# Kernel optimization log

Measured on AMD Instinct MI355X. Metric: run time of the kernel, lower is better.

The kernel has to match this reference:

```python
import jax, jax.numpy as jnp
import numpy as np

EMBED_DIM = 512
NUM_TYPES = 26
PER_TYPE = 128
NUM_CODES = NUM_TYPES * PER_TYPE
COMMIT = 0.25
TEMP = 0.07
N_TOKENS = 32768
SAMPLED_PER_TYPE = int(0.1 * PER_TYPE)  # 12


def _normalize(v, axis=-1):
    # matches F.normalize(p=2) with eps clamp
    return v / jnp.clip(jnp.linalg.norm(v, axis=axis, keepdims=True), 1e-12)


def setup_inputs() -> dict:
    key = jax.random.key(0)
    k1, k2, k3, k4 = jax.random.split(key, 4)
    x = jax.random.normal(k1, (N_TOKENS, EMBED_DIM), jnp.float32)
    Q = jax.random.randint(k2, (N_TOKENS,), 0, NUM_TYPES)
    initrange = 1.0 / EMBED_DIM
    emb = jax.random.uniform(k3, (NUM_CODES, EMBED_DIM), jnp.float32, -initrange, initrange)
    emb = _normalize(emb)  # mirrors _initialize_embeddings
    # deterministic stand-in for torch.randperm(num_per_type)[:sampled_num]
    perm = jax.random.permutation(k4, PER_TYPE)[:SAMPLED_PER_TYPE]
    sampled_indices = (jnp.arange(NUM_TYPES)[:, None] * PER_TYPE + perm[None, :]).reshape(-1)
    return {"x": x, "embeddings": emb, "Q": Q, "sampled_indices": sampled_indices}


def _code_indices(xn, embeddings, Q):
    # full [N, num_codes] squared distances, then select the 128-code slab of
    # each token's PTM type and argmin within it (equivalent to the per-type loop)
    d = ((xn ** 2).sum(-1, keepdims=True)
         + (embeddings ** 2).sum(-1)[None, :]
         - 2.0 * (xn @ embeddings.T))                      # [N, NUM_CODES]
    d = d.reshape(xn.shape[0], NUM_TYPES, PER_TYPE)
    d_sel = jnp.take_along_axis(d, Q[:, None, None], axis=1)[:, 0, :]  # [N, PER_TYPE]
    return jnp.argmin(d_sel, axis=1) + Q * PER_TYPE


def _uniform_loss(embeddings, sampled_indices):
    ne = _normalize(embeddings)
    se = ne[sampled_indices]                               # [S, D]
    sim = se @ se.T                                        # [S, S]
    labels = sampled_indices // PER_TYPE
    pos = (labels[None, :] == labels[:, None]).astype(jnp.float32)
    S = sampled_indices.shape[0]
    eye = jnp.eye(S, dtype=bool)
    sim = jnp.where(eye, -jnp.inf, sim)
    sim_exp = jnp.exp(sim / TEMP)                          # exp(-inf) = 0 kills diagonal
    sum_exp = sim_exp.sum(axis=1)
    pos_sum = (sim_exp * pos).sum(axis=1)
    return -jnp.log(pos_sum / sum_exp).mean()


def reference(x, embeddings, Q, sampled_indices):
    xn = _normalize(x)
    idx = _code_indices(xn, embeddings, Q)
    quantized = _normalize(embeddings[idx])
    q_latent = jnp.mean((quantized - jax.lax.stop_gradient(xn)) ** 2)
    e_latent = jnp.mean((xn - jax.lax.stop_gradient(quantized)) ** 2)
    loss = q_latent + COMMIT * e_latent
    uloss = _uniform_loss(embeddings, sampled_indices)
    out = xn + jax.lax.stop_gradient(quantized - xn)       # straight-through
    return out, loss, uloss, idx
```

## Files before the change

kernel.cpp:

```cpp
#include <hip/hip_runtime.h>
#include <math.h>

#define NTOK   32768
#define DIM    512
#define NTYPES 26
#define PT     128
#define NCODES 3328
#define NSAMP  312
#define INV_TEMP (1.0f / 0.07f)
#define MAXTILES 24

typedef __attribute__((ext_vector_type(8))) short short8;
typedef __attribute__((ext_vector_type(4))) float floatx4;

__device__ __forceinline__ void f2bf2(float f, unsigned short& h, unsigned short& l) {
    unsigned u = __float_as_uint(f);
    unsigned hb = (u + 0x7fffu + ((u >> 16) & 1u)) >> 16;
    h = (unsigned short)hb;
    float hf = __uint_as_float(hb << 16);
    float r = f - hf;
    unsigned u2 = __float_as_uint(r);
    l = (unsigned short)((u2 + 0x7fffu + ((u2 >> 16) & 1u)) >> 16);
}

__device__ __forceinline__ void cvt8(float4 a, float4 b, short8& h, short8& l) {
    union { short8 v; unsigned short u[8]; } H, L;
    f2bf2(a.x, H.u[0], L.u[0]); f2bf2(a.y, H.u[1], L.u[1]);
    f2bf2(a.z, H.u[2], L.u[2]); f2bf2(a.w, H.u[3], L.u[3]);
    f2bf2(b.x, H.u[4], L.u[4]); f2bf2(b.y, H.u[5], L.u[5]);
    f2bf2(b.z, H.u[6], L.u[6]); f2bf2(b.w, H.u[7], L.u[7]);
    h = H.v; l = L.v;
}

__device__ __forceinline__ void stage2(const unsigned short* g, unsigned short* l) {
    __builtin_amdgcn_global_load_lds((const __attribute__((address_space(1))) void*)g,
                                     (__attribute__((address_space(3))) void*)l, 16, 0, 0);
    __builtin_amdgcn_global_load_lds((const __attribute__((address_space(1))) void*)(g + 512),
                                     (__attribute__((address_space(3))) void*)(l + 512), 16, 0, 0);
}

__global__ __launch_bounds__(256) void k_emb(const float* __restrict__ emb,
                                             unsigned short* __restrict__ Bhg,
                                             unsigned short* __restrict__ Blg,
                                             float* __restrict__ sume,
                                             float* __restrict__ rinv,
                                             int* __restrict__ counts,
                                             float* __restrict__ accg) {
    int tid = threadIdx.x;
    if (blockIdx.x == 0) {
        if (tid < NTYPES) counts[tid] = 0;
        if (tid == 32) accg[0] = 0.0f;
        if (tid == 33) accg[1] = 0.0f;
    }
    int wv = tid >> 6, lane = tid & 63;
    int c = blockIdx.x * 4 + wv;
    const float4* row = (const float4*)(emb + (size_t)c * DIM);
    float4 v0 = row[lane * 2], v1 = row[lane * 2 + 1];
    float s = v0.x*v0.x + v0.y*v0.y + v0.z*v0.z + v0.w*v0.w
            + v1.x*v1.x + v1.y*v1.y + v1.z*v1.z + v1.w*v1.w;
    for (int m = 32; m; m >>= 1) s += __shfl_xor(s, m);
    if (lane == 0) {
        sume[c] = s;
        rinv[c] = 1.0f / fmaxf(sqrtf(s), 1e-12f);
    }
    union { short8 v; unsigned short u[8]; } hh, ll;
    f2bf2(v0.x, hh.u[0], ll.u[0]); f2bf2(v0.y, hh.u[1], ll.u[1]);
    f2bf2(v0.z, hh.u[2], ll.u[2]); f2bf2(v0.w, hh.u[3], ll.u[3]);
    f2bf2(v1.x, hh.u[4], ll.u[4]); f2bf2(v1.y, hh.u[5], ll.u[5]);
    f2bf2(v1.z, hh.u[6], ll.u[6]); f2bf2(v1.w, hh.u[7], ll.u[7]);
    int qq  = c >> 7;
    int n   = c & 127;
    int ni  = n >> 4, lcc = n & 15;
    int ks2 = lane >> 2, q4d = lane & 3;
    size_t dst = (size_t)qq * (PT * DIM)
               + (size_t)(((ks2 * 8 + ni) * 64 + q4d * 16 + lcc) * 8);
    *(short8*)(Bhg + dst) = hh.v;
    *(short8*)(Blg + dst) = ll.v;
}

__global__ __launch_bounds__(256) void k_hist(const int* __restrict__ Q,
                                              int* __restrict__ counts,
                                              int* __restrict__ rank) {
    __shared__ int lbin[NTYPES];
    __shared__ int lbase[NTYPES];
    int tid = threadIdx.x;
    if (tid < NTYPES) lbin[tid] = 0;
    __syncthreads();
    int t = blockIdx.x * 256 + tid;
    int qt = Q[t];
    int lr = atomicAdd(&lbin[qt], 1);
    __syncthreads();
    if (tid < NTYPES) lbase[tid] = atomicAdd(&counts[tid], lbin[tid]);
    __syncthreads();
    rank[t] = lbase[qt] + lr;
}

__global__ __launch_bounds__(256) void k_scatter(const int* __restrict__ Q,
                                                 const int* __restrict__ counts,
                                                 const int* __restrict__ rank,
                                                 int* __restrict__ order,
                                                 int* __restrict__ offsg) {
    __shared__ int offs[NTYPES];
    int tid = threadIdx.x;
    if (tid == 0) {
        int a = 0;
        for (int i = 0; i < NTYPES; i++) {
            offs[i] = a;
            if (blockIdx.x == 0) offsg[i] = a;
            a += counts[i];
        }
        if (blockIdx.x == 0) offsg[NTYPES] = a;
    }
    __syncthreads();
    int t = blockIdx.x * 256 + tid;
    order[offs[Q[t]] + rank[t]] = t;
}

#define KSTEP(S, NSTR, AC, AN, RESTAGE, LOADA)                                   \
  {                                                                              \
    __builtin_amdgcn_sched_barrier(0);                                           \
    asm volatile("s_waitcnt vmcnt(" NSTR ")" ::: "memory");                      \
    __builtin_amdgcn_s_barrier();                                                \
    __builtin_amdgcn_sched_barrier(0);                                           \
    if (RESTAGE) {                                                               \
      stage2(bhg + ((S) + 1) * 4096 + stoff, &Bls[((S) + 1) & 1][0][ldoff]);     \
      stage2(blg + ((S) + 1) * 4096 + stoff, &Bls[((S) + 1) & 1][1][ldoff]);     \
    }                                                                            \
    __builtin_amdgcn_sched_barrier(0);                                           \
    if (LOADA) {                                                                 \
      AN[0] = *(const float4*)(ap0 + ((S) + 1) * 32);                            \
      AN[1] = *(const float4*)(ap0 + ((S) + 1) * 32 + 4);                        \
      AN[2] = *(const float4*)(ap1 + ((S) + 1) * 32);                            \
      AN[3] = *(const float4*)(ap1 + ((S) + 1) * 32 + 4);                        \
    }                                                                            \
    {                                                                            \
      float4 r0a = AC[0], r0b = AC[1], r1a = AC[2], r1b = AC[3];                 \
      ps0 = fmaf(r0a.x, r0a.x, fmaf(r0a.y, r0a.y, fmaf(r0a.z, r0a.z, fmaf(r0a.w, r0a.w, ps0)))); \
      ps0 = fmaf(r0b.x, r0b.x, fmaf(r0b.y, r0b.y, fmaf(r0b.z, r0b.z, fmaf(r0b.w, r0b.w, ps0)))); \
      ps1 = fmaf(r1a.x, r1a.x, fmaf(r1a.y, r1a.y, fmaf(r1a.z, r1a.z, fmaf(r1a.w, r1a.w, ps1)))); \
      ps1 = fmaf(r1b.x, r1b.x, fmaf(r1b.y, r1b.y, fmaf(r1b.z, r1b.z, fmaf(r1b.w, r1b.w, ps1)))); \
      short8 ah0, al0, ah1, al1;                                                 \
      cvt8(r0a, r0b, ah0, al0);                                                  \
      cvt8(r1a, r1b, ah1, al1);                                                  \
      short8 bhf[4], blf[4];                                                     \
      _Pragma("unroll")                                                          \
      for (int ni = 0; ni < 4; ni++) {                                           \
        bhf[ni] = *(const short8*)&Bls[(S) & 1][0][(wn4 + ni) * 512 + lane8];    \
        blf[ni] = *(const short8*)&Bls[(S) & 1][1][(wn4 + ni) * 512 + lane8];    \
      }                                                                          \
      _Pragma("unroll")                                                          \
      for (int ni = 0; ni < 4; ni++) {                                           \
        acc[0][ni] = __builtin_amdgcn_mfma_f32_16x16x32_bf16(ah0, bhf[ni], acc[0][ni], 0, 0, 0); \
        acc[0][ni] = __builtin_amdgcn_mfma_f32_16x16x32_bf16(ah0, blf[ni], acc[0][ni], 0, 0, 0); \
        acc[0][ni] = __builtin_amdgcn_mfma_f32_16x16x32_bf16(al0, bhf[ni], acc[0][ni], 0, 0, 0); \
        acc[1][ni] = __builtin_amdgcn_mfma_f32_16x16x32_bf16(ah1, bhf[ni], acc[1][ni], 0, 0, 0); \
        acc[1][ni] = __builtin_amdgcn_mfma_f32_16x16x32_bf16(ah1, blf[ni], acc[1][ni], 0, 0, 0); \
        acc[1][ni] = __builtin_amdgcn_mfma_f32_16x16x32_bf16(al1, bhf[ni], acc[1][ni], 0, 0, 0); \
      }                                                                          \
    }                                                                            \
  }

__global__ __launch_bounds__(256, 3) void k_main(const float* __restrict__ x,
                                                 const float* __restrict__ emb,
                                                 const unsigned short* __restrict__ Bhg,
                                                 const unsigned short* __restrict__ Blg,
                                                 const int* __restrict__ order,
                                                 const int* __restrict__ offsg,
                                                 const float* __restrict__ sume,
                                                 const float* __restrict__ rinv,
                                                 float* __restrict__ outbuf,
                                                 float* __restrict__ idxout,
                                                 float* __restrict__ accg) {
    int q = blockIdx.x;
    int tile = blockIdx.y;
    int base = offsg[q];
    int cnt = offsg[q + 1] - base;
    int tstart = tile * 64;
    if (tstart >= cnt) return;
    int nt = min(64, cnt - tstart);

    __shared__ unsigned short Bls[2][2][4096];
    __shared__ int   toks_s[64];
    __shared__ float sume_s[128];
    __shared__ float rinv_s[128];
    __shared__ float redv[64][2];
    __shared__ int   redi[64][2];
    __shared__ int   bestc[64];

    int tid = threadIdx.x;
    int lane = tid & 63;
    int wv = tid >> 6;
    int wm = wv & 1, wn = wv >> 1;
    int lc = lane & 15, q4 = lane >> 4;
    int wn4 = wn * 4, lane8 = lane * 8;
    int stoff = wv * 1024 + lane8;
    int ldoff = wv * 1024;

    if (tid < 64) toks_s[tid] = order[base + tstart + min(tid, nt - 1)];
    if (tid < 128) {
        sume_s[tid] = sume[q * PT + tid];
        rinv_s[tid] = rinv[q * PT + tid];
    }

    int row0 = wm * 32 + lc;
    int tok0 = order[base + tstart + min(row0, nt - 1)];
    int tok1 = order[base + tstart + min(row0 + 16, nt - 1)];
    const float* ap0 = x + (size_t)tok0 * DIM + q4 * 8;
    const float* ap1 = x + (size_t)tok1 * DIM + q4 * 8;

    const unsigned short* bhg = Bhg + (size_t)q * (PT * DIM);
    const unsigned short* blg = Blg + (size_t)q * (PT * DIM);

    floatx4 acc[2][4];
#pragma unroll
    for (int mi = 0; mi < 2; mi++)
#pragma unroll
        for (int ni = 0; ni < 4; ni++)
            acc[mi][ni] = (floatx4){0.f, 0.f, 0.f, 0.f};
    float ps0 = 0.f, ps1 = 0.f;
    float4 Aa[4], Ab[4];

    stage2(bhg + stoff, &Bls[0][0][ldoff]);
    stage2(blg + stoff, &Bls[0][1][ldoff]);
    __builtin_amdgcn_sched_barrier(0);
    Aa[0] = *(const float4*)(ap0);     Aa[1] = *(const float4*)(ap0 + 4);
    Aa[2] = *(const float4*)(ap1);     Aa[3] = *(const float4*)(ap1 + 4);
    __builtin_amdgcn_sched_barrier(0);
    stage2(bhg + 4096 + stoff, &Bls[1][0][ldoff]);
    stage2(blg + 4096 + stoff, &Bls[1][1][ldoff]);
    asm volatile("s_waitcnt lgkmcnt(0)" ::: "memory");

    KSTEP(0,  "8", Aa, Ab, 0, 1)
    KSTEP(1,  "4", Ab, Aa, 1, 1)
    KSTEP(2,  "4", Aa, Ab, 1, 1)
    KSTEP(3,  "4", Ab, Aa, 1, 1)
    KSTEP(4,  "4", Aa, Ab, 1, 1)
    KSTEP(5,  "4", Ab, Aa, 1, 1)
    KSTEP(6,  "4", Aa, Ab, 1, 1)
    KSTEP(7,  "4", Ab, Aa, 1, 1)
    KSTEP(8,  "4", Aa, Ab, 1, 1)
    KSTEP(9,  "4", Ab, Aa, 1, 1)
    KSTEP(10, "4", Aa, Ab, 1, 1)
    KSTEP(11, "4", Ab, Aa, 1, 1)
    KSTEP(12, "4", Aa, Ab, 1, 1)
    KSTEP(13, "4", Ab, Aa, 1, 1)
    KSTEP(14, "4", Aa, Ab, 1, 1)
    KSTEP(15, "4", Ab, Aa, 0, 0)

    ps0 += __shfl_xor(ps0, 16); ps0 += __shfl_xor(ps0, 32);
    ps1 += __shfl_xor(ps1, 16); ps1 += __shfl_xor(ps1, 32);
    float rn0 = 1.0f / fmaxf(sqrtf(ps0), 1e-12f);
    float rn1 = 1.0f / fmaxf(sqrtf(ps1), 1e-12f);

#pragma unroll
    for (int mi = 0; mi < 2; mi++) {
#pragma unroll
        for (int r = 0; r < 4; r++) {
            int rowrel = q4 * 4 + r;
            float rn = __shfl(mi == 0 ? rn0 : rn1, rowrel);
            float rn2v = -2.0f * rn;
            float bv = 1e30f; int bc = 0;
#pragma unroll
            for (int ni = 0; ni < 4; ni++) {
                int n = wn * 64 + ni * 16 + lc;
                float d = fmaf(rn2v, acc[mi][ni][r], sume_s[n]);
                if (d < bv) { bv = d; bc = n; }
            }
#pragma unroll
            for (int mk = 1; mk <= 8; mk <<= 1) {
                float ov = __shfl_xor(bv, mk);
                int oc = __shfl_xor(bc, mk);
                if (ov < bv || (ov == bv && oc < bc)) { bv = ov; bc = oc; }
            }
            int m = wm * 32 + mi * 16 + rowrel;
            if (lc == 0) { redv[m][wn] = bv; redi[m][wn] = bc; }
        }
    }
    __syncthreads();

    if (tid < 64) {
        float v0 = redv[tid][0], v1 = redv[tid][1];
        int c = (v1 < v0) ? redi[tid][1] : redi[tid][0];
        float bvv = fminf(v0, v1);
        bestc[tid] = c;
        float term = 0.0f;
        if (tid < nt) {
            idxout[toks_s[tid]] = (float)(q * PT + c);
            term = 2.0f - (sume_s[c] - bvv) * rinv_s[c];
        }
        for (int mk = 32; mk; mk >>= 1) term += __shfl_xor(term, mk);
        if (tid == 0) atomicAdd(&accg[0], term);
    }
    __syncthreads();

    for (int t = wv; t < nt; t += 4) {
        int c = bestc[t];
        int gt = toks_s[t];
        float rv = rinv_s[c];
        const float4* er = (const float4*)(emb + (size_t)(q * PT + c) * DIM);
        float4* orow = (float4*)(outbuf + (size_t)gt * DIM);
#pragma unroll
        for (int s2 = 0; s2 < 2; s2++) {
            float4 ev = er[lane * 2 + s2];
            orow[lane * 2 + s2] = make_float4(ev.x * rv, ev.y * rv, ev.z * rv, ev.w * rv);
        }
    }
}

__global__ __launch_bounds__(256) void k_uloss(const float* __restrict__ emb,
                                               const int* __restrict__ samp,
                                               const float* __restrict__ rinv,
                                               float* __restrict__ accg) {
    __shared__ float rs[4], rp[4];
    int i = blockIdx.x;
    int tid = threadIdx.x;
    int lane = tid & 63, wv = tid >> 6;
    int ci = samp[i];
    float rvi = rinv[ci];
    int labi = ci >> 7;
    const float4* ri = (const float4*)(emb + (size_t)ci * DIM);
    float4 e0 = ri[lane * 2], e1 = ri[lane * 2 + 1];
    float sE = 0.0f, pE = 0.0f;
    for (int j0 = wv; j0 < NSAMP; j0 += 16) {
        float d[4]; int cj[4]; bool val[4];
#pragma unroll
        for (int u = 0; u < 4; u++) {
            int j = j0 + u * 4;
            val[u] = (j < NSAMP) && (j != i);
            int js = val[u] ? j : 0;
            cj[u] = samp[js];
            const float4* rj = (const float4*)(emb + (size_t)cj[u] * DIM);
            float4 f0 = rj[lane * 2], f1 = rj[lane * 2 + 1];
            d[u] = e0.x*f0.x + e0.y*f0.y + e0.z*f0.z + e0.w*f0.w
                 + e1.x*f1.x + e1.y*f1.y + e1.z*f1.z + e1.w*f1.w;
        }
#pragma unroll
        for (int mk = 32; mk; mk >>= 1)
#pragma unroll
            for (int u = 0; u < 4; u++) d[u] += __shfl_xor(d[u], mk);
#pragma unroll
        for (int u = 0; u < 4; u++) {
            float ex = val[u] ? expf(d[u] * rvi * rinv[cj[u]] * INV_TEMP) : 0.0f;
            sE += ex;
            if (val[u] && (cj[u] >> 7) == labi) pE += ex;
        }
    }
    if (lane == 0) { rs[wv] = sE; rp[wv] = pE; }
    __syncthreads();
    if (tid == 0) {
        float S = rs[0] + rs[1] + rs[2] + rs[3];
        float P = rp[0] + rp[1] + rp[2] + rp[3];
        atomicAdd(&accg[1], logf(S) - logf(P));
    }
}

__global__ void k_final(const float* __restrict__ accg, float* __restrict__ lossp) {
    lossp[0] = (1.25f / ((float)NTOK * (float)DIM)) * accg[0];
    lossp[1] = accg[1] / (float)NSAMP;
}

extern "C" void kernel_launch(void* const* d_in, const int* in_sizes, int n_in,
                              void* d_out, int out_size, void* d_ws, size_t ws_size,
                              hipStream_t stream) {
    const float* x   = (const float*)d_in[0];
    const float* emb = (const float*)d_in[1];
    const int* Q     = (const int*)d_in[2];
    const int* samp  = (const int*)d_in[3];

    float* out    = (float*)d_out;
    float* lossp  = out + (size_t)NTOK * DIM;
    float* idxout = out + (size_t)NTOK * DIM + 2;

    unsigned short* Bhg = (unsigned short*)d_ws;
    unsigned short* Blg = Bhg + (size_t)NCODES * DIM;
    float* sume  = (float*)(Blg + (size_t)NCODES * DIM);
    float* rinv  = sume + NCODES;
    int* counts  = (int*)(rinv + NCODES);
    int* offsg   = counts + NTYPES;
    int* rank    = offsg + NTYPES + 1;
    int* order   = rank + NTOK;
    float* accg  = (float*)(order + NTOK);

    k_emb<<<NCODES / 4, 256, 0, stream>>>(emb, Bhg, Blg, sume, rinv, counts, accg);
    k_hist<<<NTOK / 256, 256, 0, stream>>>(Q, counts, rank);
    k_scatter<<<NTOK / 256, 256, 0, stream>>>(Q, counts, rank, order, offsg);
    dim3 gmain(NTYPES, MAXTILES);
    k_main<<<gmain, 256, 0, stream>>>(x, emb, Bhg, Blg, order, offsg, sume, rinv, out, idxout, accg);
    k_uloss<<<NSAMP, 256, 0, stream>>>(emb, samp, rinv, accg);
    k_final<<<1, 1, 0, stream>>>(accg, lossp);
}
```

Baseline: 209.1 us.

## Halve token tile to 32 rows and deepen A-prefetch to two steps ahead

Shrinks each block's token tile from 64 to 32 rows, so every wave computes one 16-row MFMA fragment instead of two. This doubles the maximum number of tiles per type and raises the launch-bounds occupancy hint from 3 to 4 blocks. The A-operand loads move to a triple-buffered scheme that prefetches two k-steps ahead, and the vmcnt waits are retuned to match. The aim is more blocks and lower register pressure to hide latency and balance uneven per-type token counts. The cost is that each staged B slab is reused by half as many tokens, doubling codebook traffic through LDS and L2.

```diff
diff --git a/kernel.cpp b/kernel.cpp
--- a/kernel.cpp
+++ b/kernel.cpp
@@ -8,7 +8,7 @@
 #define NCODES 3328
 #define NSAMP  312
 #define INV_TEMP (1.0f / 0.07f)
-#define MAXTILES 24
+#define MAXTILES 48
 
 typedef __attribute__((ext_vector_type(8))) short short8;
 typedef __attribute__((ext_vector_type(4))) float floatx4;
@@ -116,32 +116,27 @@
     order[offs[Q[t]] + rank[t]] = t;
 }
 
-#define KSTEP(S, NSTR, AC, AN, RESTAGE, LOADA)                                   \
+#define KSTEP(S, NSTR, AC, AF, DOSTAGE, DOLOADA)                                 \
   {                                                                              \
     __builtin_amdgcn_sched_barrier(0);                                           \
     asm volatile("s_waitcnt vmcnt(" NSTR ")" ::: "memory");                      \
     __builtin_amdgcn_s_barrier();                                                \
     __builtin_amdgcn_sched_barrier(0);                                           \
-    if (RESTAGE) {                                                               \
+    if (DOSTAGE) {                                                               \
       stage2(bhg + ((S) + 1) * 4096 + stoff, &Bls[((S) + 1) & 1][0][ldoff]);     \
       stage2(blg + ((S) + 1) * 4096 + stoff, &Bls[((S) + 1) & 1][1][ldoff]);     \
     }                                                                            \
+    if (DOLOADA) {                                                               \
+      AF[0] = *(const float4*)(ap + ((S) + 2) * 32);                             \
+      AF[1] = *(const float4*)(ap + ((S) + 2) * 32 + 4);                         \
+    }                                                                            \
     __builtin_amdgcn_sched_barrier(0);                                           \
-    if (LOADA) {                                                                 \
-      AN[0] = *(const float4*)(ap0 + ((S) + 1) * 32);                            \
-      AN[1] = *(const float4*)(ap0 + ((S) + 1) * 32 + 4);                        \
-      AN[2] = *(const float4*)(ap1 + ((S) + 1) * 32);                            \
-      AN[3] = *(const float4*)(ap1 + ((S) + 1) * 32 + 4);                        \
-    }                                                                            \
     {                                                                            \
-      float4 r0a = AC[0], r0b = AC[1], r1a = AC[2], r1b = AC[3];                 \
-      ps0 = fmaf(r0a.x, r0a.x, fmaf(r0a.y, r0a.y, fmaf(r0a.z, r0a.z, fmaf(r0a.w, r0a.w, ps0)))); \
-      ps0 = fmaf(r0b.x, r0b.x, fmaf(r0b.y, r0b.y, fmaf(r0b.z, r0b.z, fmaf(r0b.w, r0b.w, ps0)))); \
-      ps1 = fmaf(r1a.x, r1a.x, fmaf(r1a.y, r1a.y, fmaf(r1a.z, r1a.z, fmaf(r1a.w, r1a.w, ps1)))); \
-      ps1 = fmaf(r1b.x, r1b.x, fmaf(r1b.y, r1b.y, fmaf(r1b.z, r1b.z, fmaf(r1b.w, r1b.w, ps1)))); \
-      short8 ah0, al0, ah1, al1;                                                 \
-      cvt8(r0a, r0b, ah0, al0);                                                  \
-      cvt8(r1a, r1b, ah1, al1);                                                  \
+      float4 a0 = AC[0], a1 = AC[1];                                             \
+      ps = fmaf(a0.x, a0.x, fmaf(a0.y, a0.y, fmaf(a0.z, a0.z, fmaf(a0.w, a0.w, ps)))); \
+      ps = fmaf(a1.x, a1.x, fmaf(a1.y, a1.y, fmaf(a1.z, a1.z, fmaf(a1.w, a1.w, ps)))); \
+      short8 ah, al;                                                             \
+      cvt8(a0, a1, ah, al);                                                      \
       short8 bhf[4], blf[4];                                                     \
       _Pragma("unroll")                                                          \
       for (int ni = 0; ni < 4; ni++) {                                           \
@@ -150,17 +145,14 @@
       }                                                                          \
       _Pragma("unroll")                                                          \
       for (int ni = 0; ni < 4; ni++) {                                           \
-        acc[0][ni] = __builtin_amdgcn_mfma_f32_16x16x32_bf16(ah0, bhf[ni], acc[0][ni], 0, 0, 0); \
-        acc[0][ni] = __builtin_amdgcn_mfma_f32_16x16x32_bf16(ah0, blf[ni], acc[0][ni], 0, 0, 0); \
-        acc[0][ni] = __builtin_amdgcn_mfma_f32_16x16x32_bf16(al0, bhf[ni], acc[0][ni], 0, 0, 0); \
-        acc[1][ni] = __builtin_amdgcn_mfma_f32_16x16x32_bf16(ah1, bhf[ni], acc[1][ni], 0, 0, 0); \
-        acc[1][ni] = __builtin_amdgcn_mfma_f32_16x16x32_bf16(ah1, blf[ni], acc[1][ni], 0, 0, 0); \
-        acc[1][ni] = __builtin_amdgcn_mfma_f32_16x16x32_bf16(al1, bhf[ni], acc[1][ni], 0, 0, 0); \
+        acc[ni] = __builtin_amdgcn_mfma_f32_16x16x32_bf16(ah, bhf[ni], acc[ni], 0, 0, 0); \
+        acc[ni] = __builtin_amdgcn_mfma_f32_16x16x32_bf16(ah, blf[ni], acc[ni], 0, 0, 0); \
+        acc[ni] = __builtin_amdgcn_mfma_f32_16x16x32_bf16(al, bhf[ni], acc[ni], 0, 0, 0); \
       }                                                                          \
     }                                                                            \
   }
 
-__global__ __launch_bounds__(256, 3) void k_main(const float* __restrict__ x,
+__global__ __launch_bounds__(256, 4) void k_main(const float* __restrict__ x,
                                                  const float* __restrict__ emb,
                                                  const unsigned short* __restrict__ Bhg,
                                                  const unsigned short* __restrict__ Blg,
@@ -175,17 +167,17 @@
     int tile = blockIdx.y;
     int base = offsg[q];
     int cnt = offsg[q + 1] - base;
-    int tstart = tile * 64;
+    int tstart = tile * 32;
     if (tstart >= cnt) return;
-    int nt = min(64, cnt - tstart);
+    int nt = min(32, cnt - tstart);
 
     __shared__ unsigned short Bls[2][2][4096];
-    __shared__ int   toks_s[64];
+    __shared__ int   toks_s[32];
     __shared__ float sume_s[128];
     __shared__ float rinv_s[128];
-    __shared__ float redv[64][2];
-    __shared__ int   redi[64][2];
-    __shared__ int   bestc[64];
+    __shared__ float redv[32][2];
+    __shared__ int   redi[32][2];
+    __shared__ int   bestc[32];
 
     int tid = threadIdx.x;
     int lane = tid & 63;
@@ -196,89 +188,75 @@
     int stoff = wv * 1024 + lane8;
     int ldoff = wv * 1024;
 
-    if (tid < 64) toks_s[tid] = order[base + tstart + min(tid, nt - 1)];
+    if (tid < 32) toks_s[tid] = order[base + tstart + min(tid, nt - 1)];
     if (tid < 128) {
         sume_s[tid] = sume[q * PT + tid];
         rinv_s[tid] = rinv[q * PT + tid];
     }
 
-    int row0 = wm * 32 + lc;
-    int tok0 = order[base + tstart + min(row0, nt - 1)];
-    int tok1 = order[base + tstart + min(row0 + 16, nt - 1)];
-    const float* ap0 = x + (size_t)tok0 * DIM + q4 * 8;
-    const float* ap1 = x + (size_t)tok1 * DIM + q4 * 8;
+    int rowA = wm * 16 + lc;
+    int tokA = order[base + tstart + min(rowA, nt - 1)];
+    const float* ap = x + (size_t)tokA * DIM + q4 * 8;
 
     const unsigned short* bhg = Bhg + (size_t)q * (PT * DIM);
     const unsigned short* blg = Blg + (size_t)q * (PT * DIM);
 
-    floatx4 acc[2][4];
-#pragma unroll
-    for (int mi = 0; mi < 2; mi++)
-#pragma unroll
-        for (int ni = 0; ni < 4; ni++)
-            acc[mi][ni] = (floatx4){0.f, 0.f, 0.f, 0.f};
-    float ps0 = 0.f, ps1 = 0.f;
-    float4 Aa[4], Ab[4];
+    floatx4 acc[4];
+#pragma unroll
+    for (int ni = 0; ni < 4; ni++) acc[ni] = (floatx4){0.f, 0.f, 0.f, 0.f};
+    float ps = 0.f;
+    float4 Aa[2], Ab[2], Ac[2];
 
     stage2(bhg + stoff, &Bls[0][0][ldoff]);
     stage2(blg + stoff, &Bls[0][1][ldoff]);
     __builtin_amdgcn_sched_barrier(0);
-    Aa[0] = *(const float4*)(ap0);     Aa[1] = *(const float4*)(ap0 + 4);
-    Aa[2] = *(const float4*)(ap1);     Aa[3] = *(const float4*)(ap1 + 4);
-    __builtin_amdgcn_sched_barrier(0);
-    stage2(bhg + 4096 + stoff, &Bls[1][0][ldoff]);
-    stage2(blg + 4096 + stoff, &Bls[1][1][ldoff]);
-    asm volatile("s_waitcnt lgkmcnt(0)" ::: "memory");
-
-    KSTEP(0,  "8", Aa, Ab, 0, 1)
-    KSTEP(1,  "4", Ab, Aa, 1, 1)
-    KSTEP(2,  "4", Aa, Ab, 1, 1)
-    KSTEP(3,  "4", Ab, Aa, 1, 1)
-    KSTEP(4,  "4", Aa, Ab, 1, 1)
-    KSTEP(5,  "4", Ab, Aa, 1, 1)
-    KSTEP(6,  "4", Aa, Ab, 1, 1)
-    KSTEP(7,  "4", Ab, Aa, 1, 1)
-    KSTEP(8,  "4", Aa, Ab, 1, 1)
-    KSTEP(9,  "4", Ab, Aa, 1, 1)
-    KSTEP(10, "4", Aa, Ab, 1, 1)
-    KSTEP(11, "4", Ab, Aa, 1, 1)
-    KSTEP(12, "4", Aa, Ab, 1, 1)
-    KSTEP(13, "4", Ab, Aa, 1, 1)
-    KSTEP(14, "4", Aa, Ab, 1, 1)
-    KSTEP(15, "4", Ab, Aa, 0, 0)
-
-    ps0 += __shfl_xor(ps0, 16); ps0 += __shfl_xor(ps0, 32);
-    ps1 += __shfl_xor(ps1, 16); ps1 += __shfl_xor(ps1, 32);
-    float rn0 = 1.0f / fmaxf(sqrtf(ps0), 1e-12f);
-    float rn1 = 1.0f / fmaxf(sqrtf(ps1), 1e-12f);
-
-#pragma unroll
-    for (int mi = 0; mi < 2; mi++) {
-#pragma unroll
-        for (int r = 0; r < 4; r++) {
-            int rowrel = q4 * 4 + r;
-            float rn = __shfl(mi == 0 ? rn0 : rn1, rowrel);
-            float rn2v = -2.0f * rn;
-            float bv = 1e30f; int bc = 0;
-#pragma unroll
-            for (int ni = 0; ni < 4; ni++) {
-                int n = wn * 64 + ni * 16 + lc;
-                float d = fmaf(rn2v, acc[mi][ni][r], sume_s[n]);
-                if (d < bv) { bv = d; bc = n; }
-            }
-#pragma unroll
-            for (int mk = 1; mk <= 8; mk <<= 1) {
-                float ov = __shfl_xor(bv, mk);
-                int oc = __shfl_xor(bc, mk);
-                if (ov < bv || (ov == bv && oc < bc)) { bv = ov; bc = oc; }
-            }
-            int m = wm * 32 + mi * 16 + rowrel;
-            if (lc == 0) { redv[m][wn] = bv; redi[m][wn] = bc; }
-        }
-    }
-    __syncthreads();
-
-    if (tid < 64) {
+    Aa[0] = *(const float4*)(ap);       Aa[1] = *(const float4*)(ap + 4);
+    Ab[0] = *(const float4*)(ap + 32);  Ab[1] = *(const float4*)(ap + 36);
+
+    KSTEP(0,  "2", Aa, Ac, 1, 1)
+    KSTEP(1,  "2", Ab, Aa, 1, 1)
+    KSTEP(2,  "2", Ac, Ab, 1, 1)
+    KSTEP(3,  "2", Aa, Ac, 1, 1)
+    KSTEP(4,  "2", Ab, Aa, 1, 1)
+    KSTEP(5,  "2", Ac, Ab, 1, 1)
+    KSTEP(6,  "2", Aa, Ac, 1, 1)
+    KSTEP(7,  "2", Ab, Aa, 1, 1)
+    KSTEP(8,  "2", Ac, Ab, 1, 1)
+    KSTEP(9,  "2", Aa, Ac, 1, 1)
+    KSTEP(10, "2", Ab, Aa, 1, 1)
+    KSTEP(11, "2", Ac, Ab, 1, 1)
+    KSTEP(12, "2", Aa, Ac, 1, 1)
+    KSTEP(13, "2", Ab, Aa, 1, 1)
+    KSTEP(14, "2", Ac, Ab, 1, 0)
+    KSTEP(15, "0", Aa, Ab, 0, 0)
+
+    ps += __shfl_xor(ps, 16);
+    ps += __shfl_xor(ps, 32);
+    float rnv = 1.0f / fmaxf(sqrtf(ps), 1e-12f);
+
+#pragma unroll
+    for (int r = 0; r < 4; r++) {
+        int rowrel = q4 * 4 + r;
+        float rn2v = -2.0f * __shfl(rnv, rowrel);
+        float bv = 1e30f; int bc = 0;
+#pragma unroll
+        for (int ni = 0; ni < 4; ni++) {
+            int n = wn * 64 + ni * 16 + lc;
+            float d = fmaf(rn2v, acc[ni][r], sume_s[n]);
+            if (d < bv) { bv = d; bc = n; }
+        }
+#pragma unroll
+        for (int mk = 1; mk <= 8; mk <<= 1) {
+            float ov = __shfl_xor(bv, mk);
+            int oc = __shfl_xor(bc, mk);
+            if (ov < bv || (ov == bv && oc < bc)) { bv = ov; bc = oc; }
+        }
+        int m = wm * 16 + rowrel;
+        if (lc == 0) { redv[m][wn] = bv; redi[m][wn] = bc; }
+    }
+    __syncthreads();
+
+    if (tid < 32) {
         float v0 = redv[tid][0], v1 = redv[tid][1];
         int c = (v1 < v0) ? redi[tid][1] : redi[tid][0];
         float bvv = fminf(v0, v1);
@@ -288,7 +266,7 @@
             idxout[toks_s[tid]] = (float)(q * PT + c);
             term = 2.0f - (sume_s[c] - bvv) * rinv_s[c];
         }
-        for (int mk = 32; mk; mk >>= 1) term += __shfl_xor(term, mk);
+        for (int mk = 16; mk; mk >>= 1) term += __shfl_xor(term, mk);
         if (tid == 0) atomicAdd(&accg[0], term);
     }
     __syncthreads();
```

After: 223.1 us. 6.7% more time.

## Triple-buffer B tiles in main GEMM and split output writes into separate kernel

Applied to the files above, without the earlier changes.

Switches the k_main K-loop from double to triple buffering of the B tiles in LDS and prefetches A two steps ahead, so more global loads are in flight per step. The per-token output row writes (gather of the chosen normalized code row) move out of k_main into a new k_out kernel that reads indices from the idx output and writes rows in token order. This shortens the tail of k_main and makes the output stores coalesced by token, but it costs more LDS per block (which may reduce occupancy), an extra kernel launch, and a re-read of the indices.

```diff
diff --git a/kernel.cpp b/kernel.cpp
--- a/kernel.cpp
+++ b/kernel.cpp
@@ -116,23 +116,21 @@
     order[offs[Q[t]] + rank[t]] = t;
 }
 
-#define KSTEP(S, NSTR, AC, AN, RESTAGE, LOADA)                                   \
+#define KSTEP(S, NSTR, AC, AF, DOSTAGE)                                          \
   {                                                                              \
     __builtin_amdgcn_sched_barrier(0);                                           \
     asm volatile("s_waitcnt vmcnt(" NSTR ")" ::: "memory");                      \
     __builtin_amdgcn_s_barrier();                                                \
     __builtin_amdgcn_sched_barrier(0);                                           \
-    if (RESTAGE) {                                                               \
-      stage2(bhg + ((S) + 1) * 4096 + stoff, &Bls[((S) + 1) & 1][0][ldoff]);     \
-      stage2(blg + ((S) + 1) * 4096 + stoff, &Bls[((S) + 1) & 1][1][ldoff]);     \
+    if (DOSTAGE) {                                                               \
+      stage2(bhg + ((S) + 2) * 4096 + stoff, &Bls[((S) + 2) % 3][0][ldoff]);     \
+      stage2(blg + ((S) + 2) * 4096 + stoff, &Bls[((S) + 2) % 3][1][ldoff]);     \
+      AF[0] = *(const float4*)(ap0 + ((S) + 2) * 32);                            \
+      AF[1] = *(const float4*)(ap0 + ((S) + 2) * 32 + 4);                        \
+      AF[2] = *(const float4*)(ap1 + ((S) + 2) * 32);                            \
+      AF[3] = *(const float4*)(ap1 + ((S) + 2) * 32 + 4);                        \
     }                                                                            \
     __builtin_amdgcn_sched_barrier(0);                                           \
-    if (LOADA) {                                                                 \
-      AN[0] = *(const float4*)(ap0 + ((S) + 1) * 32);                            \
-      AN[1] = *(const float4*)(ap0 + ((S) + 1) * 32 + 4);                        \
-      AN[2] = *(const float4*)(ap1 + ((S) + 1) * 32);                            \
-      AN[3] = *(const float4*)(ap1 + ((S) + 1) * 32 + 4);                        \
-    }                                                                            \
     {                                                                            \
       float4 r0a = AC[0], r0b = AC[1], r1a = AC[2], r1b = AC[3];                 \
       ps0 = fmaf(r0a.x, r0a.x, fmaf(r0a.y, r0a.y, fmaf(r0a.z, r0a.z, fmaf(r0a.w, r0a.w, ps0)))); \
@@ -145,8 +143,8 @@
       short8 bhf[4], blf[4];                                                     \
       _Pragma("unroll")                                                          \
       for (int ni = 0; ni < 4; ni++) {                                           \
-        bhf[ni] = *(const short8*)&Bls[(S) & 1][0][(wn4 + ni) * 512 + lane8];    \
-        blf[ni] = *(const short8*)&Bls[(S) & 1][1][(wn4 + ni) * 512 + lane8];    \
+        bhf[ni] = *(const short8*)&Bls[(S) % 3][0][(wn4 + ni) * 512 + lane8];    \
+        blf[ni] = *(const short8*)&Bls[(S) % 3][1][(wn4 + ni) * 512 + lane8];    \
       }                                                                          \
       _Pragma("unroll")                                                          \
       for (int ni = 0; ni < 4; ni++) {                                           \
@@ -161,14 +159,12 @@
   }
 
 __global__ __launch_bounds__(256, 3) void k_main(const float* __restrict__ x,
-                                                 const float* __restrict__ emb,
                                                  const unsigned short* __restrict__ Bhg,
                                                  const unsigned short* __restrict__ Blg,
                                                  const int* __restrict__ order,
                                                  const int* __restrict__ offsg,
                                                  const float* __restrict__ sume,
                                                  const float* __restrict__ rinv,
-                                                 float* __restrict__ outbuf,
                                                  float* __restrict__ idxout,
                                                  float* __restrict__ accg) {
     int q = blockIdx.x;
@@ -179,13 +175,12 @@
     if (tstart >= cnt) return;
     int nt = min(64, cnt - tstart);
 
-    __shared__ unsigned short Bls[2][2][4096];
+    __shared__ unsigned short Bls[3][2][4096];
     __shared__ int   toks_s[64];
     __shared__ float sume_s[128];
     __shared__ float rinv_s[128];
     __shared__ float redv[64][2];
     __shared__ int   redi[64][2];
-    __shared__ int   bestc[64];
 
     int tid = threadIdx.x;
     int lane = tid & 63;
@@ -218,34 +213,36 @@
         for (int ni = 0; ni < 4; ni++)
             acc[mi][ni] = (floatx4){0.f, 0.f, 0.f, 0.f};
     float ps0 = 0.f, ps1 = 0.f;
-    float4 Aa[4], Ab[4];
+    float4 Aa[4], Ab[4], Ac[4];
 
     stage2(bhg + stoff, &Bls[0][0][ldoff]);
     stage2(blg + stoff, &Bls[0][1][ldoff]);
     __builtin_amdgcn_sched_barrier(0);
-    Aa[0] = *(const float4*)(ap0);     Aa[1] = *(const float4*)(ap0 + 4);
-    Aa[2] = *(const float4*)(ap1);     Aa[3] = *(const float4*)(ap1 + 4);
+    Aa[0] = *(const float4*)(ap0);      Aa[1] = *(const float4*)(ap0 + 4);
+    Aa[2] = *(const float4*)(ap1);      Aa[3] = *(const float4*)(ap1 + 4);
     __builtin_amdgcn_sched_barrier(0);
     stage2(bhg + 4096 + stoff, &Bls[1][0][ldoff]);
     stage2(blg + 4096 + stoff, &Bls[1][1][ldoff]);
-    asm volatile("s_waitcnt lgkmcnt(0)" ::: "memory");
-
-    KSTEP(0,  "8", Aa, Ab, 0, 1)
-    KSTEP(1,  "4", Ab, Aa, 1, 1)
-    KSTEP(2,  "4", Aa, Ab, 1, 1)
-    KSTEP(3,  "4", Ab, Aa, 1, 1)
-    KSTEP(4,  "4", Aa, Ab, 1, 1)
-    KSTEP(5,  "4", Ab, Aa, 1, 1)
-    KSTEP(6,  "4", Aa, Ab, 1, 1)
-    KSTEP(7,  "4", Ab, Aa, 1, 1)
-    KSTEP(8,  "4", Aa, Ab, 1, 1)
-    KSTEP(9,  "4", Ab, Aa, 1, 1)
-    KSTEP(10, "4", Aa, Ab, 1, 1)
-    KSTEP(11, "4", Ab, Aa, 1, 1)
-    KSTEP(12, "4", Aa, Ab, 1, 1)
-    KSTEP(13, "4", Ab, Aa, 1, 1)
-    KSTEP(14, "4", Aa, Ab, 1, 1)
-    KSTEP(15, "4", Ab, Aa, 0, 0)
+    __builtin_amdgcn_sched_barrier(0);
+    Ab[0] = *(const float4*)(ap0 + 32); Ab[1] = *(const float4*)(ap0 + 36);
+    Ab[2] = *(const float4*)(ap1 + 32); Ab[3] = *(const float4*)(ap1 + 36);
+
+    KSTEP(0,  "8", Aa, Ac, 1)
+    KSTEP(1,  "8", Ab, Aa, 1)
+    KSTEP(2,  "8", Ac, Ab, 1)
+    KSTEP(3,  "8", Aa, Ac, 1)
+    KSTEP(4,  "8", Ab, Aa, 1)
+    KSTEP(5,  "8", Ac, Ab, 1)
+    KSTEP(6,  "8", Aa, Ac, 1)
+    KSTEP(7,  "8", Ab, Aa, 1)
+    KSTEP(8,  "8", Ac, Ab, 1)
+    KSTEP(9,  "8", Aa, Ac, 1)
+    KSTEP(10, "8", Ab, Aa, 1)
+    KSTEP(11, "8", Ac, Ab, 1)
+    KSTEP(12, "8", Aa, Ac, 1)
+    KSTEP(13, "8", Ab, Aa, 1)
+    KSTEP(14, "8", Ac, Ab, 0)
+    KSTEP(15, "0", Aa, Ab, 0)
 
     ps0 += __shfl_xor(ps0, 16); ps0 += __shfl_xor(ps0, 32);
     ps1 += __shfl_xor(ps1, 16); ps1 += __shfl_xor(ps1, 32);
@@ -282,7 +279,6 @@
         float v0 = redv[tid][0], v1 = redv[tid][1];
         int c = (v1 < v0) ? redi[tid][1] : redi[tid][0];
         float bvv = fminf(v0, v1);
-        bestc[tid] = c;
         float term = 0.0f;
         if (tid < nt) {
             idxout[toks_s[tid]] = (float)(q * PT + c);
@@ -291,19 +287,36 @@
         for (int mk = 32; mk; mk >>= 1) term += __shfl_xor(term, mk);
         if (tid == 0) atomicAdd(&accg[0], term);
     }
-    __syncthreads();
-
-    for (int t = wv; t < nt; t += 4) {
-        int c = bestc[t];
-        int gt = toks_s[t];
-        float rv = rinv_s[c];
-        const float4* er = (const float4*)(emb + (size_t)(q * PT + c) * DIM);
-        float4* orow = (float4*)(outbuf + (size_t)gt * DIM);
-#pragma unroll
-        for (int s2 = 0; s2 < 2; s2++) {
-            float4 ev = er[lane * 2 + s2];
-            orow[lane * 2 + s2] = make_float4(ev.x * rv, ev.y * rv, ev.z * rv, ev.w * rv);
-        }
+}
+
+__global__ __launch_bounds__(256) void k_out(const float* __restrict__ emb,
+                                             const float* __restrict__ rinv,
+                                             const float* __restrict__ idxf,
+                                             float* __restrict__ outbuf) {
+    int tid = threadIdx.x, lane = tid & 63, wv = tid >> 6;
+    int tbase = blockIdx.x * 64 + wv * 16;
+    int cL = 0; float rvL = 0.f;
+    if (lane < 16) {
+        cL = (int)idxf[tbase + lane];
+        rvL = rinv[cL];
+    }
+    const float4* er = (const float4*)emb;
+    int c0 = __shfl(cL, 0); float rv0 = __shfl(rvL, 0);
+    float4 ea = er[(size_t)c0 * 128 + lane * 2];
+    float4 eb = er[(size_t)c0 * 128 + lane * 2 + 1];
+#pragma unroll
+    for (int t = 0; t < 16; t++) {
+        float4 ca = ea, cb = eb;
+        float rv = rv0;
+        if (t < 15) {
+            int c1 = __shfl(cL, t + 1);
+            rv0 = __shfl(rvL, t + 1);
+            ea = er[(size_t)c1 * 128 + lane * 2];
+            eb = er[(size_t)c1 * 128 + lane * 2 + 1];
+        }
+        float4* orow = (float4*)(outbuf + (size_t)(tbase + t) * DIM);
+        orow[lane * 2]     = make_float4(ca.x * rv, ca.y * rv, ca.z * rv, ca.w * rv);
+        orow[lane * 2 + 1] = make_float4(cb.x * rv, cb.y * rv, cb.z * rv, cb.w * rv);
     }
 }
 
@@ -385,7 +398,8 @@
     k_hist<<<NTOK / 256, 256, 0, stream>>>(Q, counts, rank);
     k_scatter<<<NTOK / 256, 256, 0, stream>>>(Q, counts, rank, order, offsg);
     dim3 gmain(NTYPES, MAXTILES);
-    k_main<<<gmain, 256, 0, stream>>>(x, emb, Bhg, Blg, order, offsg, sume, rinv, out, idxout, accg);
+    k_main<<<gmain, 256, 0, stream>>>(x, Bhg, Blg, order, offsg, sume, rinv, idxout, accg);
+    k_out<<<NTOK / 64, 256, 0, stream>>>(emb, rinv, idxout, out);
     k_uloss<<<NSAMP, 256, 0, stream>>>(emb, samp, rinv, accg);
     k_final<<<1, 1, 0, stream>>>(accg, lossp);
 }
```

Measured after the change: 214.5 us. 1.03x slower.
